# Kernel optimization log

Hardware: AMD Instinct MI355X
Metric: run time of the kernel (lower is better)

Reference implementation:

```python
import jax, jax.numpy as jnp
import numpy as np


def _dequant(q, s, z):
    """AWQ GEMM-path dequant: W[k,n] = (q[k,n] - 8) * s[g,n] + z[g,n], g = k // group_size.
    q: [K, N] int (values in [0,16)); s, z: [K//group_size, N] float."""
    K, N = q.shape
    group_size = K // s.shape[0]
    s_full = jnp.repeat(s, group_size, axis=0)  # [K, N]
    z_full = jnp.repeat(z, group_size, axis=0)  # [K, N]
    return (q.astype(s.dtype) - 8.0) * s_full + z_full


def setup_inputs() -> dict:
    key = jax.random.key(0)
    ks = jax.random.split(key, 10)
    D, I = 4096, 11008
    G = 128
    x = jax.random.normal(ks[0], (4, 2048, D), dtype=jnp.float32)
    gate_q = jax.random.randint(ks[1], (D, I), 0, 16, dtype=jnp.int32)
    gate_s = jax.random.uniform(ks[2], (D // G, I), dtype=jnp.float32) * 0.02
    gate_z = jax.random.normal(ks[3], (D // G, I), dtype=jnp.float32) * 0.02
    up_q = jax.random.randint(ks[4], (D, I), 0, 16, dtype=jnp.int32)
    up_s = jax.random.uniform(ks[5], (D // G, I), dtype=jnp.float32) * 0.02
    up_z = jax.random.normal(ks[6], (D // G, I), dtype=jnp.float32) * 0.02
    down_q = jax.random.randint(ks[7], (I, D), 0, 16, dtype=jnp.int32)
    down_s = jax.random.uniform(ks[8], (I // G, D), dtype=jnp.float32) * 0.02
    down_z = jax.random.normal(ks[9], (I // G, D), dtype=jnp.float32) * 0.02
    return {"x": x, "gate_q": gate_q, "gate_s": gate_s, "gate_z": gate_z,
            "up_q": up_q, "up_s": up_s, "up_z": up_z,
            "down_q": down_q, "down_s": down_s, "down_z": down_z}


def reference(x, gate_q, gate_s, gate_z, up_q, up_s, up_z, down_q, down_s, down_z):
    Wg = _dequant(gate_q, gate_s, gate_z)  # [D, I]
    Wu = _dequant(up_q, up_s, up_z)        # [D, I]
    Wd = _dequant(down_q, down_s, down_z)  # [I, D]
    gate = jnp.einsum('bsd,di->bsi', x, Wg)
    up = jnp.einsum('bsd,di->bsi', x, Wu)
    h = jax.nn.silu(gate) * up
    return jnp.einsum('bsi,id->bsd', h, Wd)
```

## Files before the change

### kernel.cpp

```cpp
#include <hip/hip_runtime.h>

typedef unsigned short u16;
typedef __bf16 bf16x8 __attribute__((ext_vector_type(8)));
typedef float f32x4 __attribute__((ext_vector_type(4)));
typedef unsigned short u16x4 __attribute__((ext_vector_type(4)));
typedef unsigned short u16x8 __attribute__((ext_vector_type(8)));

__device__ __forceinline__ u16 f2bf(float f) {
    union { float f; unsigned u; } v; v.f = f;
    unsigned r = v.u + 0x7FFFu + ((v.u >> 16) & 1u);
    return (u16)(r >> 16);
}
__device__ __forceinline__ float bf2f(u16 h) {
    union { unsigned u; float f; } v; v.u = ((unsigned)h) << 16;
    return v.f;
}

__device__ __forceinline__ void gl_lds16(const void* gp, void* lp) {
    __builtin_amdgcn_global_load_lds(
        reinterpret_cast<__attribute__((address_space(1))) unsigned int*>(
            reinterpret_cast<size_t>(gp)),
        reinterpret_cast<__attribute__((address_space(3))) unsigned int*>(
            reinterpret_cast<size_t>(lp)),
        16, 0, 0);
}

__device__ __forceinline__ void swz(int bid, int nb, int& mb, int& nbk) {
    int gs  = nb << 3;
    int grp = bid / gs;
    int rem = bid - grp * gs;
    mb  = (grp << 3) + (rem & 7);
    nbk = rem >> 3;
}

__global__ __launch_bounds__(256) void xcvt(const float* __restrict__ x,
                                            u16* __restrict__ xb) {
    size_t i = ((size_t)blockIdx.x * 256 + threadIdx.x) * 8;
    float4 a = *(const float4*)(x + i);
    float4 b = *(const float4*)(x + i + 4);
    u16x8 p;
    p[0] = f2bf(a.x); p[1] = f2bf(a.y); p[2] = f2bf(a.z); p[3] = f2bf(a.w);
    p[4] = f2bf(b.x); p[5] = f2bf(b.y); p[6] = f2bf(b.z); p[7] = f2bf(b.w);
    *(u16x8*)(xb + i) = p;
}

__global__ __launch_bounds__(256) void dequant_t(
    const int* __restrict__ q, const float* __restrict__ s,
    const float* __restrict__ z, u16* __restrict__ wt, int K, int N)
{
    __shared__ u16 ls[64 * 132];
    const int n0 = blockIdx.x * 64, k0 = blockIdx.y * 128;
    const int g  = k0 >> 7;
    const int t  = threadIdx.x;
    const int n4 = (t & 15) * 4;
    const int kb = t >> 4;
    float sv[4], zv[4];
#pragma unroll
    for (int j = 0; j < 4; ++j) {
        sv[j] = s[(size_t)g * N + n0 + n4 + j];
        zv[j] = z[(size_t)g * N + n0 + n4 + j];
    }
#pragma unroll
    for (int p = 0; p < 8; ++p) {
        int kk = kb + p * 16;
        int4 qv = *(const int4*)(q + (size_t)(k0 + kk) * N + n0 + n4);
        ls[(n4 + 0) * 132 + kk] = f2bf((float)(qv.x - 8) * sv[0] + zv[0]);
        ls[(n4 + 1) * 132 + kk] = f2bf((float)(qv.y - 8) * sv[1] + zv[1]);
        ls[(n4 + 2) * 132 + kk] = f2bf((float)(qv.z - 8) * sv[2] + zv[2]);
        ls[(n4 + 3) * 132 + kk] = f2bf((float)(qv.w - 8) * sv[3] + zv[3]);
    }
    __syncthreads();
    const int r = t >> 2, c = t & 3;
    const u16* src = &ls[r * 132 + c * 32];
    u16* dst = &wt[(size_t)(n0 + r) * K + k0 + c * 32];
#pragma unroll
    for (int i = 0; i < 4; ++i) {
        u16x4 a = *(const u16x4*)(src + i * 8);
        u16x4 b = *(const u16x4*)(src + i * 8 + 4);
        u16x8 v;
        v[0] = a[0]; v[1] = a[1]; v[2] = a[2]; v[3] = a[3];
        v[4] = b[0]; v[5] = b[1]; v[6] = b[2]; v[7] = b[3];
        *(u16x8*)(dst + i * 8) = v;
    }
}

template <int EPI>
__global__ __launch_bounds__(512, 2) void gemm256(
    const u16* __restrict__ A, const u16* __restrict__ Bt,
    u16* __restrict__ gh, float* __restrict__ outp, int M, int N, int K)
{
    __shared__ __align__(16) u16 A_s[4][256 * 32];
    __shared__ __align__(16) u16 B_s[4][256 * 32];

    const int nb  = N >> 8;
    const int nwg = gridDim.x;
    const int bid = blockIdx.x;
    const int cpx = nwg >> 3;
    const int wg  = (bid & 7) * cpx + (bid >> 3);
    const int mb  = wg / nb;
    const int nbk = wg - mb * nb;
    const int m0 = mb << 8, n0 = nbk << 8;

    const int t = threadIdx.x, lane = t & 63, w = t >> 6;
    const int wm = w >> 2, wn = w & 3;
    const int lr = lane & 15;
    const int hofs = (((lane >> 4) ^ ((lane >> 1) & 3)) << 3);

    f32x4 acc[8][4] = {};

    const int NT = K >> 5;

#define STAGE_T(G, R0, TT, LS)                                              \
    {                                                                       \
        const int koff_ = (TT) * 32;                                        \
        _Pragma("unroll")                                                   \
        for (int l_ = 0; l_ < 2; ++l_) {                                    \
            int f_   = l_ * 512 + w * 64 + lane;                            \
            int row_ = f_ >> 2;                                             \
            int kc_  = (f_ & 3) ^ ((row_ >> 1) & 3);                        \
            gl_lds16((G) + (size_t)((R0) + row_) * K + koff_ + kc_ * 8,     \
                     (char*)(LS) + (size_t)(l_ * 512 + w * 64) * 16);       \
        }                                                                   \
    }

#pragma unroll
    for (int tt = 0; tt < 3; ++tt) {
        STAGE_T(A,  m0, tt, &A_s[tt][0]);
        STAGE_T(Bt, n0, tt, &B_s[tt][0]);
    }
    asm volatile("s_waitcnt vmcnt(8)" ::: "memory");
    __builtin_amdgcn_s_barrier();

    for (int tk = 0; tk < NT; ++tk) {
        const u16* Ab = &A_s[tk & 3][0];
        const u16* Bb = &B_s[tk & 3][0];
        bf16x8 av[4], bv[4];

#pragma unroll
        for (int i = 0; i < 4; ++i)
            av[i] = *(const bf16x8*)(Ab + (wm * 128 + i * 16 + lr) * 32 + hofs);
#pragma unroll
        for (int j = 0; j < 4; ++j)
            bv[j] = *(const bf16x8*)(Bb + (wn * 64 + j * 16 + lr) * 32 + hofs);
        if (tk + 3 < NT) STAGE_T(A, m0, tk + 3, &A_s[(tk + 3) & 3][0]);
        __builtin_amdgcn_s_barrier();
        __builtin_amdgcn_s_setprio(1);
#pragma unroll
        for (int i = 0; i < 4; ++i)
#pragma unroll
            for (int j = 0; j < 4; ++j)
                acc[i][j] = __builtin_amdgcn_mfma_f32_16x16x32_bf16(
                    av[i], bv[j], acc[i][j], 0, 0, 0);
        __builtin_amdgcn_s_setprio(0);
        __builtin_amdgcn_s_barrier();

#pragma unroll
        for (int i = 0; i < 4; ++i)
            av[i] = *(const bf16x8*)(Ab + (wm * 128 + 64 + i * 16 + lr) * 32 + hofs);
        if (tk + 3 < NT) STAGE_T(Bt, n0, tk + 3, &B_s[(tk + 3) & 3][0]);
        __builtin_amdgcn_s_barrier();
        __builtin_amdgcn_s_setprio(1);
#pragma unroll
        for (int i = 0; i < 4; ++i)
#pragma unroll
            for (int j = 0; j < 4; ++j)
                acc[4 + i][j] = __builtin_amdgcn_mfma_f32_16x16x32_bf16(
                    av[i], bv[j], acc[4 + i][j], 0, 0, 0);
        __builtin_amdgcn_s_setprio(0);
        if (tk < NT - 3)       asm volatile("s_waitcnt vmcnt(8)" ::: "memory");
        else if (tk == NT - 3) asm volatile("s_waitcnt vmcnt(4)" ::: "memory");
        else if (tk == NT - 2) asm volatile("s_waitcnt vmcnt(0)" ::: "memory");
        __builtin_amdgcn_s_barrier();
    }
#undef STAGE_T

    const int r0c = (lane >> 4) << 2, cc = lane & 15;
#pragma unroll
    for (int mi = 0; mi < 8; ++mi)
#pragma unroll
        for (int j = 0; j < 4; ++j)
#pragma unroll
            for (int r = 0; r < 4; ++r) {
                size_t row = (size_t)(m0 + wm * 128 + (mi >> 2) * 64 +
                                      (mi & 3) * 16 + r0c + r);
                size_t col = (size_t)(n0 + wn * 64 + j * 16 + cc);
                size_t idx = row * (size_t)N + col;
                float v = acc[mi][j][r];
                if (EPI == 0) {
                    gh[idx] = f2bf(v);
                } else if (EPI == 1) {
                    float g  = bf2f(gh[idx]);
                    float sg = g / (1.0f + __expf(-g));
                    gh[idx] = f2bf(sg * v);
                } else {
                    outp[idx] = v;
                }
            }
}

template <int AMODE, int EPI>
__global__ __launch_bounds__(256, 2) void gemm_k(
    const void* __restrict__ Ap, const u16* __restrict__ Bt,
    u16* __restrict__ ghp, float* __restrict__ outp, int M, int N, int K)
{
    __shared__ __align__(16) u16 A_s[128 * 32];
    __shared__ __align__(16) u16 B_s[128 * 32];

    const int nb = N >> 7;
    int mb, nbk; swz(blockIdx.x, nb, mb, nbk);
    const int m0 = mb << 7, n0 = nbk << 7;
    const int t = threadIdx.x, lane = t & 63, w = t >> 6;
    const int wy = w >> 1, wx = w & 1;
    const int lr = lane & 15, kq = (lane >> 4) << 3;

    f32x4 acc[4][4] = {};

    for (int kt = 0; kt < K; kt += 32) {
#pragma unroll
        for (int i = 0; i < 2; ++i) {
            int f   = (w * 2 + i) * 64 + lane;
            int row = f >> 2;
            int ko  = (f & 3) << 3;
            gl_lds16(Bt + (size_t)(n0 + row) * K + kt + ko,
                     (char*)B_s + ((w * 2 + i) << 10));
        }
        if (AMODE == 1) {
            const u16* ab = (const u16*)Ap;
#pragma unroll
            for (int i = 0; i < 2; ++i) {
                int f   = (w * 2 + i) * 64 + lane;
                int row = f >> 2;
                int ko  = (f & 3) << 3;
                gl_lds16(ab + (size_t)(m0 + row) * K + kt + ko,
                         (char*)A_s + ((w * 2 + i) << 10));
            }
        } else {
            const float* xa = (const float*)Ap;
#pragma unroll
            for (int i = 0; i < 4; ++i) {
                int c   = t + (i << 8);
                int row = c >> 3;
                int ko  = (c & 7) << 2;
                float4 v = *(const float4*)(xa + (size_t)(m0 + row) * K + kt + ko);
                u16x4 p;
                p[0] = f2bf(v.x); p[1] = f2bf(v.y); p[2] = f2bf(v.z); p[3] = f2bf(v.w);
                *(u16x4*)&A_s[row * 32 + ko] = p;
            }
        }
        __syncthreads();

        bf16x8 af[4], bv[4];
#pragma unroll
        for (int i = 0; i < 4; ++i)
            af[i] = *(const bf16x8*)&A_s[(wy * 64 + i * 16 + lr) * 32 + kq];
#pragma unroll
        for (int j = 0; j < 4; ++j)
            bv[j] = *(const bf16x8*)&B_s[(wx * 64 + j * 16 + lr) * 32 + kq];
#pragma unroll
        for (int i = 0; i < 4; ++i)
#pragma unroll
            for (int j = 0; j < 4; ++j)
                acc[i][j] = __builtin_amdgcn_mfma_f32_16x16x32_bf16(
                    af[i], bv[j], acc[i][j], 0, 0, 0);
        __syncthreads();
    }

    const int r0 = (lane >> 4) << 2, cc = lane & 15;
#pragma unroll
    for (int i = 0; i < 4; ++i)
#pragma unroll
        for (int j = 0; j < 4; ++j)
#pragma unroll
            for (int r = 0; r < 4; ++r) {
                size_t row = (size_t)(m0 + wy * 64 + i * 16 + r0 + r);
                size_t col = (size_t)(n0 + wx * 64 + j * 16 + cc);
                size_t idx = row * (size_t)N + col;
                float v = acc[i][j][r];
                if (EPI == 0) {
                    ghp[idx] = f2bf(v);
                } else if (EPI == 1) {
                    float g  = bf2f(ghp[idx]);
                    float sg = g / (1.0f + __expf(-g));
                    ghp[idx] = f2bf(sg * v);
                } else {
                    outp[idx] = v;
                }
            }
}

extern "C" void kernel_launch(void* const* d_in, const int* in_sizes, int n_in,
                              void* d_out, int out_size, void* d_ws, size_t ws_size,
                              hipStream_t stream) {
    const float* x  = (const float*)d_in[0];
    const int*   gq = (const int*)  d_in[1];
    const float* gs = (const float*)d_in[2];
    const float* gz = (const float*)d_in[3];
    const int*   uq = (const int*)  d_in[4];
    const float* us = (const float*)d_in[5];
    const float* uz = (const float*)d_in[6];
    const int*   dq = (const int*)  d_in[7];
    const float* dsc= (const float*)d_in[8];
    const float* dz = (const float*)d_in[9];
    float* out = (float*)d_out;

    const int D = 4096, I = 11008, M = 8192;
    const size_t xb_b = (size_t)M * D * 2;
    const size_t w_b  = (size_t)I * D * 2;
    const size_t gh_b = (size_t)M * I * 2;

    dim3 blk(256);
    dim3 blk5(512);

    if (ws_size >= xb_b + 2 * w_b + gh_b) {
        u16* xb = (u16*)d_ws;
        u16* Wg = (u16*)((char*)d_ws + xb_b);
        u16* Wu = (u16*)((char*)d_ws + xb_b + w_b);
        u16* gh = (u16*)((char*)d_ws + xb_b + 2 * w_b);
        u16* Wd = Wg;

        xcvt<<<(M * D) / (256 * 8), blk, 0, stream>>>(x, xb);
        dequant_t<<<dim3(I / 64, D / 128), blk, 0, stream>>>(gq, gs, gz, Wg, D, I);
        dequant_t<<<dim3(I / 64, D / 128), blk, 0, stream>>>(uq, us, uz, Wu, D, I);
        gemm256<0><<<(M / 256) * (I / 256), blk5, 0, stream>>>(xb, Wg, gh, nullptr, M, I, D);
        dequant_t<<<dim3(D / 64, I / 128), blk, 0, stream>>>(dq, dsc, dz, Wd, I, D);
        gemm256<1><<<(M / 256) * (I / 256), blk5, 0, stream>>>(xb, Wu, gh, nullptr, M, I, D);
        gemm256<2><<<(M / 256) * (D / 256), blk5, 0, stream>>>(gh, Wd, nullptr, out, M, D, I);
    } else {
        u16* Wt = (u16*)d_ws;
        u16* gh = (u16*)((char*)d_ws + w_b);

        dequant_t<<<dim3(I / 64, D / 128), blk, 0, stream>>>(gq, gs, gz, Wt, D, I);
        gemm_k<0, 0><<<(M / 128) * (I / 128), blk, 0, stream>>>(x, Wt, gh, nullptr, M, I, D);
        dequant_t<<<dim3(I / 64, D / 128), blk, 0, stream>>>(uq, us, uz, Wt, D, I);
        gemm_k<0, 1><<<(M / 128) * (I / 128), blk, 0, stream>>>(x, Wt, gh, nullptr, M, I, D);
        dequant_t<<<dim3(D / 64, I / 128), blk, 0, stream>>>(dq, dsc, dz, Wt, I, D);
        gemm_k<1, 2><<<(M / 128) * (D / 128), blk, 0, stream>>>(gh, Wt, nullptr, out, M, D, I);
    }
}
```

Before: 2.946 ms.

## Replace 256x256 GEMM tile with 128x256 tile, 4 waves, triple-buffered LDS

The main GEMM kernel moves from a 256x256 block tile with 8 waves and a 4-deep LDS ring to a 128x256 tile with 4 waves (each wave owns 128x64) and a 3-deep ring with prefetch distance 2. The intra-iteration barriers between the two MFMA halves are removed, leaving one barrier per k-step. Smaller LDS use (72KB vs 128KB) may let more blocks share a CU and doubles the grid. The cost is less A/B reuse per block, more global/L2 traffic, and a shallower prefetch that may expose load latency.

After: 3.472 ms. +17.9%, slower.

```diff
diff --git a/kernel.cpp b/kernel.cpp
--- a/kernel.cpp
+++ b/kernel.cpp
@@ -85,65 +85,73 @@
 }
 
 template <int EPI>
-__global__ __launch_bounds__(512, 2) void gemm256(
+__global__ __launch_bounds__(256, 2) void gemmC(
     const u16* __restrict__ A, const u16* __restrict__ Bt,
     u16* __restrict__ gh, float* __restrict__ outp, int M, int N, int K)
 {
-    __shared__ __align__(16) u16 A_s[4][256 * 32];
-    __shared__ __align__(16) u16 B_s[4][256 * 32];
+    __shared__ __align__(16) u16 A_s[3][128 * 32];
+    __shared__ __align__(16) u16 B_s[3][256 * 32];
 
     const int nb  = N >> 8;
+    const int bid = blockIdx.x;
     const int nwg = gridDim.x;
-    const int bid = blockIdx.x;
     const int cpx = nwg >> 3;
     const int wg  = (bid & 7) * cpx + (bid >> 3);
     const int mb  = wg / nb;
     const int nbk = wg - mb * nb;
-    const int m0 = mb << 8, n0 = nbk << 8;
+    const int m0 = mb << 7, n0 = nbk << 8;
 
     const int t = threadIdx.x, lane = t & 63, w = t >> 6;
-    const int wm = w >> 2, wn = w & 3;
     const int lr = lane & 15;
     const int hofs = (((lane >> 4) ^ ((lane >> 1) & 3)) << 3);
 
     f32x4 acc[8][4] = {};
-
     const int NT = K >> 5;
 
-#define STAGE_T(G, R0, TT, LS)                                              \
+#define STAGE_A(TT, SB)                                                     \
     {                                                                       \
-        const int koff_ = (TT) * 32;                                        \
+        const int ko_ = (TT) * 32;                                          \
         _Pragma("unroll")                                                   \
         for (int l_ = 0; l_ < 2; ++l_) {                                    \
-            int f_   = l_ * 512 + w * 64 + lane;                            \
-            int row_ = f_ >> 2;                                             \
-            int kc_  = (f_ & 3) ^ ((row_ >> 1) & 3);                        \
-            gl_lds16((G) + (size_t)((R0) + row_) * K + koff_ + kc_ * 8,     \
-                     (char*)(LS) + (size_t)(l_ * 512 + w * 64) * 16);       \
+            int f_ = l_ * 256 + t;                                          \
+            int r_ = f_ >> 2;                                               \
+            int kc_ = (f_ & 3) ^ ((r_ >> 1) & 3);                           \
+            gl_lds16(A + (size_t)(m0 + r_) * K + ko_ + kc_ * 8,             \
+                     (char*)&A_s[SB][0] + (size_t)f_ * 16);                 \
         }                                                                   \
     }
-
-#pragma unroll
-    for (int tt = 0; tt < 3; ++tt) {
-        STAGE_T(A,  m0, tt, &A_s[tt][0]);
-        STAGE_T(Bt, n0, tt, &B_s[tt][0]);
-    }
-    asm volatile("s_waitcnt vmcnt(8)" ::: "memory");
+#define STAGE_B(TT, SB)                                                     \
+    {                                                                       \
+        const int ko_ = (TT) * 32;                                          \
+        _Pragma("unroll")                                                   \
+        for (int l_ = 0; l_ < 4; ++l_) {                                    \
+            int f_ = l_ * 256 + t;                                          \
+            int r_ = f_ >> 2;                                               \
+            int kc_ = (f_ & 3) ^ ((r_ >> 1) & 3);                           \
+            gl_lds16(Bt + (size_t)(n0 + r_) * K + ko_ + kc_ * 8,            \
+                     (char*)&B_s[SB][0] + (size_t)f_ * 16);                 \
+        }                                                                   \
+    }
+
+    STAGE_A(0, 0); STAGE_B(0, 0);
+    STAGE_A(1, 1); STAGE_B(1, 1);
+    asm volatile("s_waitcnt vmcnt(6)" ::: "memory");
     __builtin_amdgcn_s_barrier();
 
+    int cb = 0;
     for (int tk = 0; tk < NT; ++tk) {
-        const u16* Ab = &A_s[tk & 3][0];
-        const u16* Bb = &B_s[tk & 3][0];
+        const u16* Ab = &A_s[cb][0];
+        const u16* Bb = &B_s[cb][0];
+        const int sb = (cb + 2 >= 3) ? cb - 1 : cb + 2;
         bf16x8 av[4], bv[4];
 
 #pragma unroll
-        for (int i = 0; i < 4; ++i)
-            av[i] = *(const bf16x8*)(Ab + (wm * 128 + i * 16 + lr) * 32 + hofs);
-#pragma unroll
         for (int j = 0; j < 4; ++j)
-            bv[j] = *(const bf16x8*)(Bb + (wn * 64 + j * 16 + lr) * 32 + hofs);
-        if (tk + 3 < NT) STAGE_T(A, m0, tk + 3, &A_s[(tk + 3) & 3][0]);
-        __builtin_amdgcn_s_barrier();
+            bv[j] = *(const bf16x8*)(Bb + (w * 64 + j * 16 + lr) * 32 + hofs);
+#pragma unroll
+        for (int i = 0; i < 4; ++i)
+            av[i] = *(const bf16x8*)(Ab + (i * 16 + lr) * 32 + hofs);
+        if (tk + 2 < NT) STAGE_A(tk + 2, sb);
         __builtin_amdgcn_s_setprio(1);
 #pragma unroll
         for (int i = 0; i < 4; ++i)
@@ -152,13 +160,11 @@
                 acc[i][j] = __builtin_amdgcn_mfma_f32_16x16x32_bf16(
                     av[i], bv[j], acc[i][j], 0, 0, 0);
         __builtin_amdgcn_s_setprio(0);
-        __builtin_amdgcn_s_barrier();
-
-#pragma unroll
-        for (int i = 0; i < 4; ++i)
-            av[i] = *(const bf16x8*)(Ab + (wm * 128 + 64 + i * 16 + lr) * 32 + hofs);
-        if (tk + 3 < NT) STAGE_T(Bt, n0, tk + 3, &B_s[(tk + 3) & 3][0]);
-        __builtin_amdgcn_s_barrier();
+
+#pragma unroll
+        for (int i = 0; i < 4; ++i)
+            av[i] = *(const bf16x8*)(Ab + (64 + i * 16 + lr) * 32 + hofs);
+        if (tk + 2 < NT) STAGE_B(tk + 2, sb);
         __builtin_amdgcn_s_setprio(1);
 #pragma unroll
         for (int i = 0; i < 4; ++i)
@@ -167,12 +173,14 @@
                 acc[4 + i][j] = __builtin_amdgcn_mfma_f32_16x16x32_bf16(
                     av[i], bv[j], acc[4 + i][j], 0, 0, 0);
         __builtin_amdgcn_s_setprio(0);
-        if (tk < NT - 3)       asm volatile("s_waitcnt vmcnt(8)" ::: "memory");
-        else if (tk == NT - 3) asm volatile("s_waitcnt vmcnt(4)" ::: "memory");
-        else if (tk == NT - 2) asm volatile("s_waitcnt vmcnt(0)" ::: "memory");
+
+        if (tk + 2 < NT)      asm volatile("s_waitcnt vmcnt(6)" ::: "memory");
+        else if (tk + 1 < NT) asm volatile("s_waitcnt vmcnt(0)" ::: "memory");
         __builtin_amdgcn_s_barrier();
-    }
-#undef STAGE_T
+        cb = (cb + 1 >= 3) ? 0 : cb + 1;
+    }
+#undef STAGE_A
+#undef STAGE_B
 
     const int r0c = (lane >> 4) << 2, cc = lane & 15;
 #pragma unroll
@@ -181,9 +189,8 @@
         for (int j = 0; j < 4; ++j)
 #pragma unroll
             for (int r = 0; r < 4; ++r) {
-                size_t row = (size_t)(m0 + wm * 128 + (mi >> 2) * 64 +
-                                      (mi & 3) * 16 + r0c + r);
-                size_t col = (size_t)(n0 + wn * 64 + j * 16 + cc);
+                size_t row = (size_t)(m0 + (mi >> 2) * 64 + (mi & 3) * 16 + r0c + r);
+                size_t col = (size_t)(n0 + w * 64 + j * 16 + cc);
                 size_t idx = row * (size_t)N + col;
                 float v = acc[mi][j][r];
                 if (EPI == 0) {
@@ -309,7 +316,6 @@
     const size_t gh_b = (size_t)M * I * 2;
 
     dim3 blk(256);
-    dim3 blk5(512);
 
     if (ws_size >= xb_b + 2 * w_b + gh_b) {
         u16* xb = (u16*)d_ws;
@@ -321,10 +327,10 @@
         xcvt<<<(M * D) / (256 * 8), blk, 0, stream>>>(x, xb);
         dequant_t<<<dim3(I / 64, D / 128), blk, 0, stream>>>(gq, gs, gz, Wg, D, I);
         dequant_t<<<dim3(I / 64, D / 128), blk, 0, stream>>>(uq, us, uz, Wu, D, I);
-        gemm256<0><<<(M / 256) * (I / 256), blk5, 0, stream>>>(xb, Wg, gh, nullptr, M, I, D);
+        gemmC<0><<<(M / 128) * (I / 256), blk, 0, stream>>>(xb, Wg, gh, nullptr, M, I, D);
         dequant_t<<<dim3(D / 64, I / 128), blk, 0, stream>>>(dq, dsc, dz, Wd, I, D);
-        gemm256<1><<<(M / 256) * (I / 256), blk5, 0, stream>>>(xb, Wu, gh, nullptr, M, I, D);
-        gemm256<2><<<(M / 256) * (D / 256), blk5, 0, stream>>>(gh, Wd, nullptr, out, M, D, I);
+        gemmC<1><<<(M / 128) * (I / 256), blk, 0, stream>>>(xb, Wu, gh, nullptr, M, I, D);
+        gemmC<2><<<(M / 128) * (D / 256), blk, 0, stream>>>(gh, Wd, nullptr, out, M, D, I);
     } else {
         u16* Wt = (u16*)d_ws;
         u16* gh = (u16*)((char*)d_ws + w_b);
```

## Restructure 256x256 GEMM into 8-phase ping-pong schedule with K=64 tiles

Applied to the files above, without the earlier changes.

Replaces the 4-stage K=32 pipelined GEMM with a double-buffered K=64 scheme. The A and B tiles are split into half-tiles, and each iteration runs eight phases that interleave LDS fragment reads, global-to-LDS staging of the next half-tiles, and MFMA blocks, separated by barriers. The goal is better overlap of memory traffic with MFMA work and fewer waits per unit of K. In exchange it adds more barriers and more intricate vmcnt accounting, which could stall or race if the staging order is wrong.

Result: no change. 2.902 ms (-1.5%).

```diff
diff --git a/kernel.cpp b/kernel.cpp
--- a/kernel.cpp
+++ b/kernel.cpp
@@ -24,6 +24,8 @@
             reinterpret_cast<size_t>(lp)),
         16, 0, 0);
 }
+
+#define BAR() { asm volatile("" ::: "memory"); __builtin_amdgcn_s_barrier(); asm volatile("" ::: "memory"); }
 
 __device__ __forceinline__ void swz(int bid, int nb, int& mb, int& nbk) {
     int gs  = nb << 3;
@@ -85,107 +87,148 @@
 }
 
 template <int EPI>
-__global__ __launch_bounds__(512, 2) void gemm256(
+__global__ __launch_bounds__(512, 2) void gemm8p(
     const u16* __restrict__ A, const u16* __restrict__ Bt,
     u16* __restrict__ gh, float* __restrict__ outp, int M, int N, int K)
 {
-    __shared__ __align__(16) u16 A_s[4][256 * 32];
-    __shared__ __align__(16) u16 B_s[4][256 * 32];
+    __shared__ __align__(16) u16 As[2][2][128 * 64];
+    __shared__ __align__(16) u16 Bs[2][2][128 * 64];
 
     const int nb  = N >> 8;
-    const int nwg = gridDim.x;
-    const int bid = blockIdx.x;
+    const int bid = blockIdx.x, nwg = gridDim.x;
     const int cpx = nwg >> 3;
     const int wg  = (bid & 7) * cpx + (bid >> 3);
-    const int mb  = wg / nb;
-    const int nbk = wg - mb * nb;
+    const int mb  = wg / nb, nbk = wg - mb * nb;
     const int m0 = mb << 8, n0 = nbk << 8;
 
     const int t = threadIdx.x, lane = t & 63, w = t >> 6;
     const int wm = w >> 2, wn = w & 3;
     const int lr = lane & 15;
-    const int hofs = (((lane >> 4) ^ ((lane >> 1) & 3)) << 3);
+    const int qofs = (((lane >> 4) ^ ((lr >> 1) & 3)) << 3);
 
     f32x4 acc[8][4] = {};
-
-    const int NT = K >> 5;
-
-#define STAGE_T(G, R0, TT, LS)                                              \
+    bf16x8 av[4][2], bv[2][2];
+
+    const int NT = K >> 6;
+    const int NI = NT >> 1;
+
+#define STG_A(TT, DB, H)                                                    \
     {                                                                       \
-        const int koff_ = (TT) * 32;                                        \
+        const int ko_ = (TT) << 6;                                          \
         _Pragma("unroll")                                                   \
         for (int l_ = 0; l_ < 2; ++l_) {                                    \
-            int f_   = l_ * 512 + w * 64 + lane;                            \
-            int row_ = f_ >> 2;                                             \
-            int kc_  = (f_ & 3) ^ ((row_ >> 1) & 3);                        \
-            gl_lds16((G) + (size_t)((R0) + row_) * K + koff_ + kc_ * 8,     \
-                     (char*)(LS) + (size_t)(l_ * 512 + w * 64) * 16);       \
+            int f_  = l_ * 512 + t;                                         \
+            int r_  = f_ >> 3, s_ = f_ & 7;                                 \
+            int c_  = (s_ & 4) | ((s_ & 3) ^ ((r_ >> 1) & 3));              \
+            int gr_ = ((r_ >> 6) << 7) + ((H) << 6) + (r_ & 63);            \
+            gl_lds16(A + (size_t)(m0 + gr_) * K + ko_ + c_ * 8,             \
+                     (char*)&As[DB][H][0] + f_ * 16);                       \
         }                                                                   \
     }
-
-#pragma unroll
-    for (int tt = 0; tt < 3; ++tt) {
-        STAGE_T(A,  m0, tt, &A_s[tt][0]);
-        STAGE_T(Bt, n0, tt, &B_s[tt][0]);
-    }
-    asm volatile("s_waitcnt vmcnt(8)" ::: "memory");
-    __builtin_amdgcn_s_barrier();
-
-    for (int tk = 0; tk < NT; ++tk) {
-        const u16* Ab = &A_s[tk & 3][0];
-        const u16* Bb = &B_s[tk & 3][0];
-        bf16x8 av[4], bv[4];
-
-#pragma unroll
-        for (int i = 0; i < 4; ++i)
-            av[i] = *(const bf16x8*)(Ab + (wm * 128 + i * 16 + lr) * 32 + hofs);
-#pragma unroll
-        for (int j = 0; j < 4; ++j)
-            bv[j] = *(const bf16x8*)(Bb + (wn * 64 + j * 16 + lr) * 32 + hofs);
-        if (tk + 3 < NT) STAGE_T(A, m0, tk + 3, &A_s[(tk + 3) & 3][0]);
-        __builtin_amdgcn_s_barrier();
-        __builtin_amdgcn_s_setprio(1);
-#pragma unroll
-        for (int i = 0; i < 4; ++i)
-#pragma unroll
-            for (int j = 0; j < 4; ++j)
-                acc[i][j] = __builtin_amdgcn_mfma_f32_16x16x32_bf16(
-                    av[i], bv[j], acc[i][j], 0, 0, 0);
-        __builtin_amdgcn_s_setprio(0);
-        __builtin_amdgcn_s_barrier();
-
-#pragma unroll
-        for (int i = 0; i < 4; ++i)
-            av[i] = *(const bf16x8*)(Ab + (wm * 128 + 64 + i * 16 + lr) * 32 + hofs);
-        if (tk + 3 < NT) STAGE_T(Bt, n0, tk + 3, &B_s[(tk + 3) & 3][0]);
-        __builtin_amdgcn_s_barrier();
-        __builtin_amdgcn_s_setprio(1);
-#pragma unroll
-        for (int i = 0; i < 4; ++i)
-#pragma unroll
-            for (int j = 0; j < 4; ++j)
-                acc[4 + i][j] = __builtin_amdgcn_mfma_f32_16x16x32_bf16(
-                    av[i], bv[j], acc[4 + i][j], 0, 0, 0);
-        __builtin_amdgcn_s_setprio(0);
-        if (tk < NT - 3)       asm volatile("s_waitcnt vmcnt(8)" ::: "memory");
-        else if (tk == NT - 3) asm volatile("s_waitcnt vmcnt(4)" ::: "memory");
-        else if (tk == NT - 2) asm volatile("s_waitcnt vmcnt(0)" ::: "memory");
-        __builtin_amdgcn_s_barrier();
-    }
-#undef STAGE_T
+#define STG_B(TT, DB, H)                                                    \
+    {                                                                       \
+        const int ko_ = (TT) << 6;                                          \
+        _Pragma("unroll")                                                   \
+        for (int l_ = 0; l_ < 2; ++l_) {                                    \
+            int f_  = l_ * 512 + t;                                         \
+            int r_  = f_ >> 3, s_ = f_ & 7;                                 \
+            int c_  = (s_ & 4) | ((s_ & 3) ^ ((r_ >> 1) & 3));              \
+            int gr_ = ((r_ >> 5) << 6) + ((H) << 5) + (r_ & 31);            \
+            gl_lds16(Bt + (size_t)(n0 + gr_) * K + ko_ + c_ * 8,            \
+                     (char*)&Bs[DB][H][0] + f_ * 16);                       \
+        }                                                                   \
+    }
+#define LDA(DB, H)                                                          \
+    _Pragma("unroll")                                                       \
+    for (int fa_ = 0; fa_ < 4; ++fa_)                                       \
+        _Pragma("unroll")                                                   \
+        for (int kk_ = 0; kk_ < 2; ++kk_)                                   \
+            av[fa_][kk_] = *(const bf16x8*)&As[DB][H][                      \
+                (wm * 64 + fa_ * 16 + lr) * 64 + kk_ * 32 + qofs];
+#define LDB(DB, H)                                                          \
+    _Pragma("unroll")                                                       \
+    for (int bb_ = 0; bb_ < 2; ++bb_)                                       \
+        _Pragma("unroll")                                                   \
+        for (int kk_ = 0; kk_ < 2; ++kk_)                                   \
+            bv[bb_][kk_] = *(const bf16x8*)&Bs[DB][H][                      \
+                (wn * 32 + bb_ * 16 + lr) * 64 + kk_ * 32 + qofs];
+#define MM(AB, BB)                                                          \
+    __builtin_amdgcn_s_setprio(1);                                          \
+    _Pragma("unroll")                                                       \
+    for (int fa_ = 0; fa_ < 4; ++fa_)                                       \
+        _Pragma("unroll")                                                   \
+        for (int bb_ = 0; bb_ < 2; ++bb_)                                   \
+            _Pragma("unroll")                                               \
+            for (int kk_ = 0; kk_ < 2; ++kk_)                               \
+                acc[(AB) + fa_][(BB) + bb_] =                               \
+                    __builtin_amdgcn_mfma_f32_16x16x32_bf16(                \
+                        av[fa_][kk_], bv[bb_][kk_],                         \
+                        acc[(AB) + fa_][(BB) + bb_], 0, 0, 0);              \
+    __builtin_amdgcn_s_setprio(0);
+
+    STG_A(0, 0, 0); STG_B(0, 0, 0); STG_A(0, 0, 1); STG_B(0, 0, 1);
+    STG_A(1, 1, 0); STG_B(1, 1, 1);
+    asm volatile("s_waitcnt vmcnt(4)" ::: "memory");
+    BAR();
+
+    for (int it = 0; it < NI; ++it) {
+        const int T = it << 1;
+        const bool more = (it < NI - 1);
+
+        LDA(0, 0); LDB(0, 0);
+        STG_B(T + 1, 1, 0);
+        BAR(); MM(0, 0); BAR();
+
+        LDB(0, 1);
+        STG_A(T + 1, 1, 1);
+        BAR(); MM(0, 2); BAR();
+
+        LDA(0, 1);
+        if (more) STG_A(T + 2, 0, 0);
+        BAR(); MM(4, 2); BAR();
+
+        LDB(0, 0);
+        if (more) STG_B(T + 2, 0, 1);
+        BAR(); MM(4, 0);
+        if (more) { asm volatile("s_waitcnt vmcnt(4)" ::: "memory"); }
+        else      { asm volatile("s_waitcnt vmcnt(0)" ::: "memory"); }
+        BAR();
+
+        LDA(1, 0); LDB(1, 0);
+        if (more) STG_B(T + 2, 0, 0);
+        BAR(); MM(0, 0); BAR();
+
+        LDB(1, 1);
+        if (more) STG_A(T + 2, 0, 1);
+        BAR(); MM(0, 2); BAR();
+
+        LDA(1, 1);
+        if (more) STG_A(T + 3, 1, 0);
+        BAR(); MM(4, 2); BAR();
+
+        LDB(1, 0);
+        if (more) STG_B(T + 3, 1, 1);
+        BAR(); MM(4, 0);
+        if (more) { asm volatile("s_waitcnt vmcnt(4)" ::: "memory"); }
+        BAR();
+    }
+#undef STG_A
+#undef STG_B
+#undef LDA
+#undef LDB
+#undef MM
 
     const int r0c = (lane >> 4) << 2, cc = lane & 15;
 #pragma unroll
-    for (int mi = 0; mi < 8; ++mi)
-#pragma unroll
-        for (int j = 0; j < 4; ++j)
+    for (int a = 0; a < 8; ++a)
+#pragma unroll
+        for (int b = 0; b < 4; ++b)
 #pragma unroll
             for (int r = 0; r < 4; ++r) {
-                size_t row = (size_t)(m0 + wm * 128 + (mi >> 2) * 64 +
-                                      (mi & 3) * 16 + r0c + r);
-                size_t col = (size_t)(n0 + wn * 64 + j * 16 + cc);
+                size_t row = (size_t)(m0 + wm * 128 + a * 16 + r0c + r);
+                size_t col = (size_t)(n0 + wn * 64 + b * 16 + cc);
                 size_t idx = row * (size_t)N + col;
-                float v = acc[mi][j][r];
+                float v = acc[a][b][r];
                 if (EPI == 0) {
                     gh[idx] = f2bf(v);
                 } else if (EPI == 1) {
@@ -321,10 +364,10 @@
         xcvt<<<(M * D) / (256 * 8), blk, 0, stream>>>(x, xb);
         dequant_t<<<dim3(I / 64, D / 128), blk, 0, stream>>>(gq, gs, gz, Wg, D, I);
         dequant_t<<<dim3(I / 64, D / 128), blk, 0, stream>>>(uq, us, uz, Wu, D, I);
-        gemm256<0><<<(M / 256) * (I / 256), blk5, 0, stream>>>(xb, Wg, gh, nullptr, M, I, D);
+        gemm8p<0><<<(M / 256) * (I / 256), blk5, 0, stream>>>(xb, Wg, gh, nullptr, M, I, D);
         dequant_t<<<dim3(D / 64, I / 128), blk, 0, stream>>>(dq, dsc, dz, Wd, I, D);
-        gemm256<1><<<(M / 256) * (I / 256), blk5, 0, stream>>>(xb, Wu, gh, nullptr, M, I, D);
-        gemm256<2><<<(M / 256) * (D / 256), blk5, 0, stream>>>(gh, Wd, nullptr, out, M, D, I);
+        gemm8p<1><<<(M / 256) * (I / 256), blk5, 0, stream>>>(xb, Wu, gh, nullptr, M, I, D);
+        gemm8p<2><<<(M / 256) * (D / 256), blk5, 0, stream>>>(gh, Wd, nullptr, out, M, D, I);
     } else {
         u16* Wt = (u16*)d_ws;
         u16* gh = (u16*)((char*)d_ws + w_b);
```
